# Performance work log

Measured on AMD Instinct MI355X. Metric: run time of the kernel, lower is better.

## Reference

```python
import jax, jax.numpy as jnp
import numpy as np

B, D, H, W = 2, 256, 64, 64
NH = 4
EPS = 1e-5


def _ln(x, g, b):
    # LayerNorm over channel dim of NCHW tensor (matches permute->LN(C)->permute)
    mu = jnp.mean(x, axis=1, keepdims=True)
    var = jnp.mean((x - mu) ** 2, axis=1, keepdims=True)
    xn = (x - mu) * jax.lax.rsqrt(var + EPS)
    return xn * g[None, :, None, None] + b[None, :, None, None]


def _conv1x1(x, w, b):
    # w: (out_c, in_c)
    return jnp.einsum('bchw,oc->bohw', x, w) + b[None, :, None, None]


def _dwconv3x3(x, w, b):
    # depthwise 3x3, w: (C, 1, 3, 3)
    y = jax.lax.conv_general_dilated(
        x, w, window_strides=(1, 1), padding='SAME',
        dimension_numbers=('NCHW', 'OIHW', 'NCHW'), feature_group_count=D)
    return y + b[None, :, None, None]


def setup_inputs() -> dict:
    key = jax.random.key(0)
    ks = jax.random.split(key, 12)
    sc = 0.02

    def n(k, shape):
        return jax.random.normal(k, shape, dtype=jnp.float32) * sc

    return {
        'image_embedding': jax.random.normal(ks[0], (B, D, H, W), dtype=jnp.float32),
        'guide': jax.random.normal(ks[1], (B, D, H, W), dtype=jnp.float32),
        'ln1_g': jnp.ones((D,), jnp.float32), 'ln1_b': jnp.zeros((D,), jnp.float32),
        'ln2_g': jnp.ones((D,), jnp.float32), 'ln2_b': jnp.zeros((D,), jnp.float32),
        'qw1': n(ks[2], (D, D)), 'qb1': jnp.zeros((D,), jnp.float32),
        'qw2': n(ks[3], (D, 1, 3, 3)), 'qb2': jnp.zeros((D,), jnp.float32),
        'kw1': n(ks[4], (D, D)), 'kb1': jnp.zeros((D,), jnp.float32),
        'kw2': n(ks[5], (D, 1, 3, 3)), 'kb2': jnp.zeros((D,), jnp.float32),
        'vw1': n(ks[6], (D, D)), 'vb1': jnp.zeros((D,), jnp.float32),
        'vw2': n(ks[7], (D, 1, 3, 3)), 'vb2': jnp.zeros((D,), jnp.float32),
        'ow': n(ks[8], (D, D)), 'ob': jnp.zeros((D,), jnp.float32),
    }


def reference(image_embedding, guide, ln1_g, ln1_b, ln2_g, ln2_b,
              qw1, qb1, qw2, qb2, kw1, kb1, kw2, kb2,
              vw1, vb1, vw2, vb2, ow, ob):
    residual = image_embedding
    x = _ln(image_embedding, ln1_g, ln1_b)
    g = _ln(guide, ln2_g, ln2_b)

    q = _dwconv3x3(_conv1x1(x, qw1, qb1), qw2, qb2)
    k = _dwconv3x3(_conv1x1(g, kw1, kb1), kw2, kb2)
    v = _dwconv3x3(_conv1x1(g, vw1, vb1), vw2, vb2)

    hd = D // NH
    scale = hd ** -0.5

    def to_heads(t):  # (B,C,H,W) -> (B, NH, HW, hd)
        return t.reshape(B, NH, hd, H * W).transpose(0, 1, 3, 2)

    q = to_heads(q) * scale
    k = to_heads(k)
    v = to_heads(v)

    attn = jax.nn.softmax(jnp.einsum('bhnd,bhmd->bhnm', q, k), axis=-1)
    out = jnp.einsum('bhnm,bhmd->bhnd', attn, v)
    out = out.transpose(0, 1, 3, 2).reshape(B, D, H, W)
    out = _conv1x1(out, ow, ob)
    return residual + out
```

## Files before the change

kernel.cpp:

```cpp
#include <hip/hip_runtime.h>
#include <cstdint>
#include <cstddef>

typedef unsigned short u16;
typedef unsigned int u32;
typedef __attribute__((ext_vector_type(8))) short short8;
typedef __attribute__((ext_vector_type(4))) float f32x4;

#define CD 256
#define HWD 4096
#define NHD 4
#define HDD 64

static __device__ __forceinline__ u16 f2b(float f) {
    u32 u = __builtin_bit_cast(u32, f);
    return (u16)((u + 0x7fffu + ((u >> 16) & 1u)) >> 16);
}
static __device__ __forceinline__ float b2f(u16 h) {
    return __builtin_bit_cast(float, (u32)h << 16);
}
static __device__ __forceinline__ u32 pk2(float a, float b) {
    return (u32)f2b(a) | ((u32)f2b(b) << 16);
}
static __device__ __forceinline__ u32 pk2r(float a, float b) {
    u32 ua = __builtin_bit_cast(u32, a) + 0x8000u;
    u32 ub = __builtin_bit_cast(u32, b) + 0x8000u;
    return (ua >> 16) | (ub & 0xffff0000u);
}
static __device__ __forceinline__ float fexp2(float x) {
#if __has_builtin(__builtin_amdgcn_exp2f)
    return __builtin_amdgcn_exp2f(x);
#else
    return __expf(x * 0.69314718056f);
#endif
}
static __device__ __forceinline__ void async16(const void* g, void* l) {
    __builtin_amdgcn_global_load_lds(
        (const __attribute__((address_space(1))) unsigned int*)g,
        (__attribute__((address_space(3))) unsigned int*)l,
        16, 0, 0);
}

__global__ __launch_bounds__(256) void ln_transpose(
    const float* __restrict__ x0, const float* __restrict__ x1,
    const float* __restrict__ g0, const float* __restrict__ b0,
    const float* __restrict__ g1, const float* __restrict__ b1,
    u16* __restrict__ out0, u16* __restrict__ out1)
{
    int bid = blockIdx.x;
    int t = bid >> 8, b = (bid >> 7) & 1, p0 = (bid & 127) << 5;
    const float* x = t ? x1 : x0;
    const float* g = t ? g1 : g0;
    const float* bb = t ? b1 : b0;
    u16* out = t ? out1 : out0;

    int tid = threadIdx.x;
    int tx = tid & 31, ty = tid >> 5;
    const float* xb = x + (size_t)b * CD * HWD + p0 + tx;

    __shared__ float red[2][8][32];
    __shared__ u16 T[256][33];

    float s = 0.f, sq = 0.f;
    #pragma unroll 8
    for (int i = 0; i < 32; ++i) {
        float v = xb[(size_t)(ty * 32 + i) * HWD];
        s += v; sq += v * v;
    }
    red[0][ty][tx] = s; red[1][ty][tx] = sq;
    __syncthreads();
    float st = 0.f, sqt = 0.f;
    #pragma unroll
    for (int j = 0; j < 8; ++j) { st += red[0][j][tx]; sqt += red[1][j][tx]; }
    float mean = st * (1.f / 256.f);
    float var = sqt * (1.f / 256.f) - mean * mean;
    float rstd = rsqrtf(var + 1e-5f);

    #pragma unroll 8
    for (int i = 0; i < 32; ++i) {
        int c = ty * 32 + i;
        float v = (xb[(size_t)c * HWD] - mean) * rstd * g[c] + bb[c];
        T[c][tx] = f2b(v);
    }
    __syncthreads();

    #pragma unroll
    for (int pass = 0; pass < 4; ++pass) {
        int idx = pass * 256 + tid;
        int p = idx >> 5, cs = (idx & 31) * 8;
        u16 tmp[8];
        #pragma unroll
        for (int j = 0; j < 8; ++j) tmp[j] = T[cs + j][p];
        *(uint4*)&out[((size_t)b * HWD + p0 + p) * CD + cs] = *(const uint4*)tmp;
    }
}

__global__ __launch_bounds__(256) void qkv_gemm(
    const u16* __restrict__ xT, const u16* __restrict__ gT,
    const float* __restrict__ qw1, const float* __restrict__ qb1,
    const float* __restrict__ kw1, const float* __restrict__ kb1,
    const float* __restrict__ vw1, const float* __restrict__ vb1,
    u16* __restrict__ q1, u16* __restrict__ k1, u16* __restrict__ v1)
{
    int z = blockIdx.z;
    int mm = z >> 1, b = z & 1;
    const u16* X    = (mm == 0) ? xT : gT;
    const float* W  = (mm == 0) ? qw1 : (mm == 1) ? kw1 : vw1;
    const float* Bi = (mm == 0) ? qb1 : (mm == 1) ? kb1 : vb1;
    u16* Y          = (mm == 0) ? q1 : (mm == 1) ? k1 : v1;

    int n0 = blockIdx.x * 128;
    int p0 = blockIdx.y * 64;

    __shared__ u16 As[64][40];
    __shared__ u16 Bs[128][40];

    int tid = threadIdx.x;
    int lane = tid & 63, w = tid >> 6;
    int wm = w >> 1, wn = w & 1;
    int l15 = lane & 15, quad = lane >> 4;

    f32x4 acc[2][4];
    #pragma unroll
    for (int mi = 0; mi < 2; ++mi)
        #pragma unroll
        for (int nj = 0; nj < 4; ++nj)
            acc[mi][nj] = (f32x4){0.f, 0.f, 0.f, 0.f};

    const u16* Xb = X + (size_t)b * HWD * CD;

    int arow = tid >> 2, aseg = (tid & 3) * 8;
    const u16* agp = Xb + (size_t)(p0 + arow) * CD + aseg;
    int brow = tid >> 1, bkh = (tid & 1) * 16;
    const float* wgp = W + (size_t)(n0 + brow) * CD + bkh;

    uint4 ra = *(const uint4*)(agp);
    float4 rw0 = ((const float4*)wgp)[0], rw1 = ((const float4*)wgp)[1];
    float4 rw2 = ((const float4*)wgp)[2], rw3 = ((const float4*)wgp)[3];

    for (int kt = 0; kt < 8; ++kt) {
        __syncthreads();
        *(uint4*)&As[arow][aseg] = ra;
        {
            uint4 qa, qb;
            qa.x = pk2(rw0.x, rw0.y); qa.y = pk2(rw0.z, rw0.w);
            qa.z = pk2(rw1.x, rw1.y); qa.w = pk2(rw1.z, rw1.w);
            qb.x = pk2(rw2.x, rw2.y); qb.y = pk2(rw2.z, rw2.w);
            qb.z = pk2(rw3.x, rw3.y); qb.w = pk2(rw3.z, rw3.w);
            *(uint4*)&Bs[brow][bkh] = qa;
            *(uint4*)&Bs[brow][bkh + 8] = qb;
        }
        if (kt < 7) {
            ra = *(const uint4*)(agp + (kt + 1) * 32);
            const float* wg2 = wgp + (kt + 1) * 32;
            rw0 = ((const float4*)wg2)[0]; rw1 = ((const float4*)wg2)[1];
            rw2 = ((const float4*)wg2)[2]; rw3 = ((const float4*)wg2)[3];
        }
        __syncthreads();

        short8 af[2], bf[4];
        #pragma unroll
        for (int mi = 0; mi < 2; ++mi)
            af[mi] = *(const short8*)&As[wm * 32 + mi * 16 + l15][quad * 8];
        #pragma unroll
        for (int nj = 0; nj < 4; ++nj)
            bf[nj] = *(const short8*)&Bs[wn * 64 + nj * 16 + l15][quad * 8];
        #pragma unroll
        for (int mi = 0; mi < 2; ++mi)
            #pragma unroll
            for (int nj = 0; nj < 4; ++nj)
                acc[mi][nj] = __builtin_amdgcn_mfma_f32_16x16x32_bf16(
                    af[mi], bf[nj], acc[mi][nj], 0, 0, 0);
    }

    u16* Yb = Y + (size_t)b * HWD * CD;
    float bias[4];
    #pragma unroll
    for (int nj = 0; nj < 4; ++nj)
        bias[nj] = Bi[n0 + wn * 64 + nj * 16 + l15];
    #pragma unroll
    for (int mi = 0; mi < 2; ++mi) {
        #pragma unroll
        for (int r = 0; r < 4; ++r) {
            int p = p0 + wm * 32 + mi * 16 + quad * 4 + r;
            #pragma unroll
            for (int nj = 0; nj < 4; ++nj) {
                int ch = n0 + wn * 64 + nj * 16 + l15;
                Yb[(size_t)p * CD + ch] = f2b(acc[mi][nj][r] + bias[nj]);
            }
        }
    }
}

__global__ __launch_bounds__(256) void dwconv_nc(
    const u16* __restrict__ q1, const u16* __restrict__ k1, const u16* __restrict__ v1,
    const float* __restrict__ qw2, const float* __restrict__ qb2,
    const float* __restrict__ kw2, const float* __restrict__ kb2,
    const float* __restrict__ vw2, const float* __restrict__ vb2,
    u16* __restrict__ Q, u16* __restrict__ K, u16* __restrict__ Vt)
{
    int bid = blockIdx.x;
    int which = bid >> 9;
    int b = (bid >> 8) & 1;
    int p0 = (bid & 255) * 16;

    const u16* in = ((which == 0) ? q1 : (which == 1) ? k1 : v1) + (size_t)b * HWD * CD;
    const float* wsrc = (which == 0) ? qw2 : (which == 1) ? kw2 : vw2;
    const float* bsrc = (which == 0) ? qb2 : (which == 1) ? kb2 : vb2;
    float oscale = (which == 0) ? 0.18033688011112042f : 1.0f;

    int c = threadIdx.x;
    float w9[9];
    #pragma unroll
    for (int j = 0; j < 9; ++j) w9[j] = wsrc[c * 9 + j];
    float bias = bsrc[c];

    int h = p0 >> 6, w0 = p0 & 63;

    float accv[16];
    #pragma unroll
    for (int pi = 0; pi < 16; ++pi) accv[pi] = bias;

    #pragma unroll
    for (int dh = 0; dh < 3; ++dh) {
        int hh = h + dh - 1;
        if (hh < 0 || hh >= 64) continue;
        const u16* rp = in + ((size_t)hh * 64) * CD + c;
        float r[18];
        r[0] = (w0 > 0) ? b2f(rp[(size_t)(w0 - 1) * CD]) : 0.f;
        #pragma unroll
        for (int j = 1; j <= 16; ++j)
            r[j] = b2f(rp[(size_t)(w0 - 1 + j) * CD]);
        r[17] = (w0 < 48) ? b2f(rp[(size_t)(w0 + 16) * CD]) : 0.f;

        float wa = w9[dh * 3 + 0], wb = w9[dh * 3 + 1], wc = w9[dh * 3 + 2];
        #pragma unroll
        for (int pi = 0; pi < 16; ++pi)
            accv[pi] += wa * r[pi] + wb * r[pi + 1] + wc * r[pi + 2];
    }

    if (which == 2) {
        u32 w8[8];
        #pragma unroll
        for (int j = 0; j < 8; ++j) w8[j] = pk2(accv[2 * j], accv[2 * j + 1]);
        uint4* dst = (uint4*)(Vt + ((size_t)(b * CD + c)) * HWD + p0);
        dst[0] = make_uint4(w8[0], w8[1], w8[2], w8[3]);
        dst[1] = make_uint4(w8[4], w8[5], w8[6], w8[7]);
    } else {
        u16* out = ((which == 0) ? Q : K) + (size_t)b * HWD * CD;
        #pragma unroll
        for (int pi = 0; pi < 16; ++pi)
            out[(size_t)(p0 + pi) * CD + c] = f2b(accv[pi] * oscale);
    }
}

__global__ __launch_bounds__(256, 2) void attn_kernel(
    const u16* __restrict__ Q, const u16* __restrict__ K,
    const u16* __restrict__ Vt, u16* __restrict__ Opart,
    float* __restrict__ Psum)
{
    int qt = blockIdx.x;
    int bh = blockIdx.y;
    int ks = blockIdx.z;
    int b = bh >> 2, nh = bh & 3;

    __shared__ u16 Ks_[2][64 * 64];
    __shared__ u16 Vs_[2][64 * 64];
    __shared__ u16 Ps[256 * 64];

    int tid = threadIdx.x;
    int lane = tid & 63, w = tid >> 6;
    int l15 = lane & 15, quad = lane >> 4;
    int sw = l15 & 7;

    const u16* Qb = Q + ((size_t)b * HWD) * CD + nh * 64;
    const u16* Kb = K + ((size_t)b * HWD) * CD + nh * 64;
    const u16* Vb = Vt + ((size_t)bh * HDD) * HWD;

    short8 qf[4][2];
    #pragma unroll
    for (int qi = 0; qi < 4; ++qi) {
        const u16* qrow = Qb + (size_t)(qt * 256 + w * 64 + qi * 16 + l15) * CD + quad * 8;
        qf[qi][0] = *(const short8*)(qrow);
        qf[qi][1] = *(const short8*)(qrow + 32);
    }

    int rr = lane >> 3;
    int gseg = (lane & 7) ^ rr;
    const u16* kgb = Kb + (size_t)(ks * 1024 + w * 16 + rr) * CD + gseg * 8;
    const u16* vgb = Vb + (size_t)(w * 16 + rr) * HWD + ks * 1024 + gseg * 8;

    f32x4 acc_o[4][4];
    float psum[4] = {0.f, 0.f, 0.f, 0.f};
    #pragma unroll
    for (int qi = 0; qi < 4; ++qi)
        #pragma unroll
        for (int dj = 0; dj < 4; ++dj)
            acc_o[qi][dj] = (f32x4){0.f, 0.f, 0.f, 0.f};

    #pragma unroll
    for (int j = 0; j < 2; ++j) {
        async16(kgb + (size_t)(j * 8) * CD, &Ks_[0][(w * 16 + j * 8) * 64]);
        async16(vgb + (size_t)(j * 8) * HWD, &Vs_[0][(w * 16 + j * 8) * 64]);
    }

    for (int it = 0; it < 16; ++it) {
        int cur = it & 1;
        __syncthreads();
        if (it + 1 < 16) {
            int nxt = cur ^ 1;
            #pragma unroll
            for (int j = 0; j < 2; ++j) {
                async16(kgb + (size_t)((it + 1) * 64 + j * 8) * CD,
                        &Ks_[nxt][(w * 16 + j * 8) * 64]);
                async16(vgb + (size_t)(j * 8) * HWD + (it + 1) * 64,
                        &Vs_[nxt][(w * 16 + j * 8) * 64]);
            }
        }

        short8 kf[4][2];
        #pragma unroll
        for (int nj = 0; nj < 4; ++nj)
            #pragma unroll
            for (int kk = 0; kk < 2; ++kk)
                kf[nj][kk] = *(const short8*)&Ks_[cur][(nj * 16 + l15) * 64 +
                                                      (((kk * 4 + quad) ^ sw) << 3)];

        #pragma unroll
        for (int qi = 0; qi < 4; ++qi) {
            f32x4 st[4];
            #pragma unroll
            for (int nj = 0; nj < 4; ++nj) st[nj] = (f32x4){0.f, 0.f, 0.f, 0.f};
            #pragma unroll
            for (int kk = 0; kk < 2; ++kk)
                #pragma unroll
                for (int nj = 0; nj < 4; ++nj)
                    st[nj] = __builtin_amdgcn_mfma_f32_16x16x32_bf16(
                        kf[nj][kk], qf[qi][kk], st[nj], 0, 0, 0);

            int prow = (w * 64 + qi * 16 + l15) * 64;
            #pragma unroll
            for (int nj = 0; nj < 4; ++nj) {
                float e0 = fexp2(st[nj][0]);
                float e1 = fexp2(st[nj][1]);
                float e2 = fexp2(st[nj][2]);
                float e3 = fexp2(st[nj][3]);
                psum[qi] += (e0 + e1) + (e2 + e3);
                uint2 pw;
                pw.x = pk2r(e0, e1);
                pw.y = pk2r(e2, e3);
                int pcol = (((nj * 2 + (quad >> 1)) ^ sw) << 3) + (quad & 1) * 4;
                *(uint2*)&Ps[prow + pcol] = pw;
            }
        }

        short8 vf[4][2];
        #pragma unroll
        for (int dj = 0; dj < 4; ++dj)
            #pragma unroll
            for (int kk = 0; kk < 2; ++kk)
                vf[dj][kk] = *(const short8*)&Vs_[cur][(dj * 16 + l15) * 64 +
                                                      (((kk * 4 + quad) ^ sw) << 3)];

        #pragma unroll
        for (int kk = 0; kk < 2; ++kk)
            #pragma unroll
            for (int qi = 0; qi < 4; ++qi) {
                short8 pf = *(const short8*)&Ps[(w * 64 + qi * 16 + l15) * 64 +
                                                (((kk * 4 + quad) ^ sw) << 3)];
                #pragma unroll
                for (int dj = 0; dj < 4; ++dj)
                    acc_o[qi][dj] = __builtin_amdgcn_mfma_f32_16x16x32_bf16(
                        pf, vf[dj][kk], acc_o[qi][dj], 0, 0, 0);
            }
    }

    u16* Ob = Opart + (((size_t)ks * 8 + bh) * HWD) * HDD;
    #pragma unroll
    for (int qi = 0; qi < 4; ++qi)
        #pragma unroll
        for (int dj = 0; dj < 4; ++dj)
            #pragma unroll
            for (int r = 0; r < 4; ++r) {
                int n = qt * 256 + w * 64 + qi * 16 + quad * 4 + r;
                Ob[(size_t)n * HDD + dj * 16 + l15] = f2b(acc_o[qi][dj][r]);
            }

    float* Pb = Psum + ((size_t)ks * 8 + bh) * HWD + qt * 256 + w * 64;
    #pragma unroll
    for (int qi = 0; qi < 4; ++qi) {
        float s = psum[qi];
        s += __shfl_xor(s, 16);
        s += __shfl_xor(s, 32);
        if (quad == 0) Pb[qi * 16 + l15] = s;
    }
}

__global__ __launch_bounds__(256) void out_gemm(
    const float* __restrict__ W, const float* __restrict__ Bi,
    const u16* __restrict__ Opart, const float* __restrict__ Psum,
    const float* __restrict__ residual, float* __restrict__ out)
{
    int b = blockIdx.z;
    int m0 = blockIdx.y * 64;
    int n0 = blockIdx.x * 64;

    __shared__ u16 As[64][40];
    __shared__ u16 Bs[64][40];

    int tid = threadIdx.x;
    int lane = tid & 63, w = tid >> 6;
    int wm = w >> 1, wn = w & 1;
    int l15 = lane & 15, quad = lane >> 4;

    f32x4 acc[2][2];
    #pragma unroll
    for (int mi = 0; mi < 2; ++mi)
        #pragma unroll
        for (int nj = 0; nj < 2; ++nj)
            acc[mi][nj] = (f32x4){0.f, 0.f, 0.f, 0.f};

    int arow = tid >> 2, aseg = (tid & 3) * 8;
    const float* wgp = W + (size_t)(m0 + arow) * CD + aseg;
    int brow = tid >> 2, bseg = (tid & 3) * 8;
    int pn = n0 + brow;

    float4 rw0 = ((const float4*)wgp)[0], rw1 = ((const float4*)wgp)[1];

    uint4 ro[4]; float rinv;
    {
        int c = bseg;
        int bh = b * 4 + (c >> 6), d0 = c & 63;
        float p = 0.f;
        #pragma unroll
        for (int s = 0; s < 4; ++s) {
            ro[s] = *(const uint4*)&Opart[(((size_t)s * 8 + bh) * HWD + pn) * HDD + d0];
            p += Psum[((size_t)s * 8 + bh) * HWD + pn];
        }
        rinv = 1.f / p;
    }

    for (int kt = 0; kt < 8; ++kt) {
        __syncthreads();
        {
            uint4 qa;
            qa.x = pk2(rw0.x, rw0.y); qa.y = pk2(rw0.z, rw0.w);
            qa.z = pk2(rw1.x, rw1.y); qa.w = pk2(rw1.z, rw1.w);
            *(uint4*)&As[arow][aseg] = qa;
        }
        {
            float v[8];
            #pragma unroll
            for (int j = 0; j < 8; ++j) v[j] = 0.f;
            #pragma unroll
            for (int s = 0; s < 4; ++s) {
                u16 t[8];
                *(uint4*)t = ro[s];
                #pragma unroll
                for (int j = 0; j < 8; ++j) v[j] += b2f(t[j]);
            }
            uint4 bb;
            bb.x = pk2(v[0] * rinv, v[1] * rinv);
            bb.y = pk2(v[2] * rinv, v[3] * rinv);
            bb.z = pk2(v[4] * rinv, v[5] * rinv);
            bb.w = pk2(v[6] * rinv, v[7] * rinv);
            *(uint4*)&Bs[brow][bseg] = bb;
        }
        if (kt < 7) {
            const float* wg2 = wgp + (kt + 1) * 32;
            rw0 = ((const float4*)wg2)[0]; rw1 = ((const float4*)wg2)[1];
            int c = (kt + 1) * 32 + bseg;
            int bh = b * 4 + (c >> 6), d0 = c & 63;
            float p = 0.f;
            #pragma unroll
            for (int s = 0; s < 4; ++s) {
                ro[s] = *(const uint4*)&Opart[(((size_t)s * 8 + bh) * HWD + pn) * HDD + d0];
                p += Psum[((size_t)s * 8 + bh) * HWD + pn];
            }
            rinv = 1.f / p;
        }
        __syncthreads();

        short8 af[2], bf[2];
        #pragma unroll
        for (int mi = 0; mi < 2; ++mi)
            af[mi] = *(const short8*)&As[wm * 32 + mi * 16 + l15][quad * 8];
        #pragma unroll
        for (int nj = 0; nj < 2; ++nj)
            bf[nj] = *(const short8*)&Bs[wn * 32 + nj * 16 + l15][quad * 8];
        #pragma unroll
        for (int mi = 0; mi < 2; ++mi)
            #pragma unroll
            for (int nj = 0; nj < 2; ++nj)
                acc[mi][nj] = __builtin_amdgcn_mfma_f32_16x16x32_bf16(
                    af[mi], bf[nj], acc[mi][nj], 0, 0, 0);
    }

    #pragma unroll
    for (int mi = 0; mi < 2; ++mi) {
        int mb = m0 + wm * 32 + mi * 16 + quad * 4;
        #pragma unroll
        for (int r = 0; r < 4; ++r) {
            float bias = Bi[mb + r];
            const float* res = residual + (size_t)(b * CD + mb + r) * HWD;
            float* o = out + (size_t)(b * CD + mb + r) * HWD;
            #pragma unroll
            for (int nj = 0; nj < 2; ++nj) {
                int n = n0 + wn * 32 + nj * 16 + l15;
                o[n] = acc[mi][nj][r] + bias + res[n];
            }
        }
    }
}

extern "C" void kernel_launch(void* const* d_in, const int* in_sizes, int n_in,
                              void* d_out, int out_size, void* d_ws, size_t ws_size,
                              hipStream_t stream) {
    (void)in_sizes; (void)n_in; (void)out_size; (void)ws_size;

    const float* image = (const float*)d_in[0];
    const float* guide = (const float*)d_in[1];
    const float* ln1_g = (const float*)d_in[2];
    const float* ln1_b = (const float*)d_in[3];
    const float* ln2_g = (const float*)d_in[4];
    const float* ln2_b = (const float*)d_in[5];
    const float* qw1 = (const float*)d_in[6];
    const float* qb1 = (const float*)d_in[7];
    const float* qw2 = (const float*)d_in[8];
    const float* qb2 = (const float*)d_in[9];
    const float* kw1 = (const float*)d_in[10];
    const float* kb1 = (const float*)d_in[11];
    const float* kw2 = (const float*)d_in[12];
    const float* kb2 = (const float*)d_in[13];
    const float* vw1 = (const float*)d_in[14];
    const float* vb1 = (const float*)d_in[15];
    const float* vw2 = (const float*)d_in[16];
    const float* vb2 = (const float*)d_in[17];
    const float* ow  = (const float*)d_in[18];
    const float* ob  = (const float*)d_in[19];
    float* out = (float*)d_out;

    char* ws = (char*)d_ws;
    u16* xT    = (u16*)(ws + (size_t)0  * (1 << 20));
    u16* gT    = (u16*)(ws + (size_t)4  * (1 << 20));
    u16* q1    = (u16*)(ws + (size_t)8  * (1 << 20));
    u16* k1    = (u16*)(ws + (size_t)12 * (1 << 20));
    u16* v1    = (u16*)(ws + (size_t)16 * (1 << 20));
    u16* Qh    = (u16*)(ws + (size_t)20 * (1 << 20));
    u16* Kh    = (u16*)(ws + (size_t)24 * (1 << 20));
    u16* Vt    = (u16*)(ws + (size_t)28 * (1 << 20));
    u16*   Opart = (u16*)(ws + (size_t)0  * (1 << 20));
    float* Psum  = (float*)(ws + (size_t)18 * (1 << 20));

    ln_transpose<<<dim3(512), dim3(256), 0, stream>>>(
        image, guide, ln1_g, ln1_b, ln2_g, ln2_b, xT, gT);

    qkv_gemm<<<dim3(2, 64, 6), dim3(256), 0, stream>>>(
        xT, gT, qw1, qb1, kw1, kb1, vw1, vb1, q1, k1, v1);

    dwconv_nc<<<dim3(1536), dim3(256), 0, stream>>>(
        q1, k1, v1, qw2, qb2, kw2, kb2, vw2, vb2, Qh, Kh, Vt);

    attn_kernel<<<dim3(16, 8, 4), dim3(256), 0, stream>>>(Qh, Kh, Vt, Opart, Psum);

    out_gemm<<<dim3(64, 4, 2), dim3(256), 0, stream>>>(
        ow, ob, Opart, Psum, image, out);
}
```

Before: 182.1 us.

## Switch attention to 32x32 MFMA with register-resident P via permlane swap

Rewrites the attention inner loop to use 32x32x16 bf16 MFMAs, with each wave owning 32 query rows instead of 64. The exponentiated scores are converted with v_cvt_pk_bf16_f32 and rearranged with permlane32_swap, so they feed the PV MFMA straight from registers and the LDS P staging buffer is gone. Dropping the 32KB P buffer and using fewer query rows per block allows four blocks per CU and doubles the grid. In exchange, K/V tiles are reloaded from global memory by twice as many blocks, and correctness depends on the swapped lane layout matching the MFMA operand layout.

```diff
diff --git a/kernel.cpp b/kernel.cpp
--- a/kernel.cpp
+++ b/kernel.cpp
@@ -6,6 +6,8 @@
 typedef unsigned int u32;
 typedef __attribute__((ext_vector_type(8))) short short8;
 typedef __attribute__((ext_vector_type(4))) float f32x4;
+typedef __attribute__((ext_vector_type(16))) float f32x16;
+typedef __attribute__((ext_vector_type(2))) unsigned int u32x2;
 
 #define CD 256
 #define HWD 4096
@@ -21,11 +23,6 @@
 }
 static __device__ __forceinline__ u32 pk2(float a, float b) {
     return (u32)f2b(a) | ((u32)f2b(b) << 16);
-}
-static __device__ __forceinline__ u32 pk2r(float a, float b) {
-    u32 ua = __builtin_bit_cast(u32, a) + 0x8000u;
-    u32 ub = __builtin_bit_cast(u32, b) + 0x8000u;
-    return (ua >> 16) | (ub & 0xffff0000u);
 }
 static __device__ __forceinline__ float fexp2(float x) {
 #if __has_builtin(__builtin_amdgcn_exp2f)
@@ -33,6 +30,14 @@
 #else
     return __expf(x * 0.69314718056f);
 #endif
+}
+static __device__ __forceinline__ u32 cvtpk(float lo, float hi) {
+    u32 r;
+    asm("v_cvt_pk_bf16_f32 %0, %1, %2" : "=v"(r) : "v"(lo), "v"(hi));
+    return r;
+}
+static __device__ __forceinline__ u32x2 plswap(u32 a, u32 b) {
+    return __builtin_amdgcn_permlane32_swap(a, b, false, false);
 }
 static __device__ __forceinline__ void async16(const void* g, void* l) {
     __builtin_amdgcn_global_load_lds(
@@ -254,7 +259,7 @@
     }
 }
 
-__global__ __launch_bounds__(256, 2) void attn_kernel(
+__global__ __launch_bounds__(256, 4) void attn_kernel(
     const u16* __restrict__ Q, const u16* __restrict__ K,
     const u16* __restrict__ Vt, u16* __restrict__ Opart,
     float* __restrict__ Psum)
@@ -266,37 +271,34 @@
 
     __shared__ u16 Ks_[2][64 * 64];
     __shared__ u16 Vs_[2][64 * 64];
-    __shared__ u16 Ps[256 * 64];
 
     int tid = threadIdx.x;
     int lane = tid & 63, w = tid >> 6;
-    int l15 = lane & 15, quad = lane >> 4;
-    int sw = l15 & 7;
+    int l31 = lane & 31, h = lane >> 5;
+    int sw = l31 & 7;
 
     const u16* Qb = Q + ((size_t)b * HWD) * CD + nh * 64;
     const u16* Kb = K + ((size_t)b * HWD) * CD + nh * 64;
     const u16* Vb = Vt + ((size_t)bh * HDD) * HWD;
 
-    short8 qf[4][2];
-    #pragma unroll
-    for (int qi = 0; qi < 4; ++qi) {
-        const u16* qrow = Qb + (size_t)(qt * 256 + w * 64 + qi * 16 + l15) * CD + quad * 8;
-        qf[qi][0] = *(const short8*)(qrow);
-        qf[qi][1] = *(const short8*)(qrow + 32);
-    }
+    int q0 = qt * 128 + w * 32;
+
+    short8 qf[4];
+    #pragma unroll
+    for (int si = 0; si < 4; ++si)
+        qf[si] = *(const short8*)(Qb + (size_t)(q0 + l31) * CD + si * 16 + h * 8);
 
     int rr = lane >> 3;
     int gseg = (lane & 7) ^ rr;
     const u16* kgb = Kb + (size_t)(ks * 1024 + w * 16 + rr) * CD + gseg * 8;
     const u16* vgb = Vb + (size_t)(w * 16 + rr) * HWD + ks * 1024 + gseg * 8;
 
-    f32x4 acc_o[4][4];
-    float psum[4] = {0.f, 0.f, 0.f, 0.f};
-    #pragma unroll
-    for (int qi = 0; qi < 4; ++qi)
-        #pragma unroll
-        for (int dj = 0; dj < 4; ++dj)
-            acc_o[qi][dj] = (f32x4){0.f, 0.f, 0.f, 0.f};
+    f32x16 acc[2];
+    #pragma unroll
+    for (int db = 0; db < 2; ++db)
+        #pragma unroll
+        for (int r = 0; r < 16; ++r) acc[db][r] = 0.f;
+    float psum = 0.f;
 
     #pragma unroll
     for (int j = 0; j < 2; ++j) {
@@ -318,82 +320,65 @@
             }
         }
 
-        short8 kf[4][2];
-        #pragma unroll
-        for (int nj = 0; nj < 4; ++nj)
-            #pragma unroll
-            for (int kk = 0; kk < 2; ++kk)
-                kf[nj][kk] = *(const short8*)&Ks_[cur][(nj * 16 + l15) * 64 +
-                                                      (((kk * 4 + quad) ^ sw) << 3)];
-
-        #pragma unroll
-        for (int qi = 0; qi < 4; ++qi) {
-            f32x4 st[4];
-            #pragma unroll
-            for (int nj = 0; nj < 4; ++nj) st[nj] = (f32x4){0.f, 0.f, 0.f, 0.f};
-            #pragma unroll
-            for (int kk = 0; kk < 2; ++kk)
-                #pragma unroll
-                for (int nj = 0; nj < 4; ++nj)
-                    st[nj] = __builtin_amdgcn_mfma_f32_16x16x32_bf16(
-                        kf[nj][kk], qf[qi][kk], st[nj], 0, 0, 0);
-
-            int prow = (w * 64 + qi * 16 + l15) * 64;
-            #pragma unroll
-            for (int nj = 0; nj < 4; ++nj) {
-                float e0 = fexp2(st[nj][0]);
-                float e1 = fexp2(st[nj][1]);
-                float e2 = fexp2(st[nj][2]);
-                float e3 = fexp2(st[nj][3]);
-                psum[qi] += (e0 + e1) + (e2 + e3);
-                uint2 pw;
-                pw.x = pk2r(e0, e1);
-                pw.y = pk2r(e2, e3);
-                int pcol = (((nj * 2 + (quad >> 1)) ^ sw) << 3) + (quad & 1) * 4;
-                *(uint2*)&Ps[prow + pcol] = pw;
+        #pragma unroll
+        for (int kb = 0; kb < 2; ++kb) {
+            short8 kf[4];
+            #pragma unroll
+            for (int si = 0; si < 4; ++si)
+                kf[si] = *(const short8*)&Ks_[cur][(kb * 32 + l31) * 64 +
+                                                   (((si * 2 + h) ^ sw) << 3)];
+            f32x16 st;
+            #pragma unroll
+            for (int r = 0; r < 16; ++r) st[r] = 0.f;
+            #pragma unroll
+            for (int si = 0; si < 4; ++si)
+                st = __builtin_amdgcn_mfma_f32_32x32x16_bf16(
+                    kf[si], qf[si], st, 0, 0, 0);
+
+            float e[16];
+            #pragma unroll
+            for (int r = 0; r < 16; ++r) e[r] = fexp2(st[r]);
+            #pragma unroll
+            for (int r = 0; r < 16; r += 4)
+                psum += (e[r] + e[r + 1]) + (e[r + 2] + e[r + 3]);
+
+            u32 wv[8];
+            #pragma unroll
+            for (int m = 0; m < 8; ++m) wv[m] = cvtpk(e[2 * m], e[2 * m + 1]);
+            u32x2 s02 = plswap(wv[0], wv[2]);
+            u32x2 s13 = plswap(wv[1], wv[3]);
+            u32x2 s46 = plswap(wv[4], wv[6]);
+            u32x2 s57 = plswap(wv[5], wv[7]);
+            union { u32 u[4]; short8 s8; } p0_, p1_;
+            p0_.u[0] = s02.x; p0_.u[1] = s13.x; p0_.u[2] = s02.y; p0_.u[3] = s13.y;
+            p1_.u[0] = s46.x; p1_.u[1] = s57.x; p1_.u[2] = s46.y; p1_.u[3] = s57.y;
+
+            #pragma unroll
+            for (int db = 0; db < 2; ++db) {
+                short8 vf0 = *(const short8*)&Vs_[cur][(db * 32 + l31) * 64 +
+                                 ((((kb * 2 + 0) * 2 + h) ^ sw) << 3)];
+                acc[db] = __builtin_amdgcn_mfma_f32_32x32x16_bf16(
+                    p0_.s8, vf0, acc[db], 0, 0, 0);
+                short8 vf1 = *(const short8*)&Vs_[cur][(db * 32 + l31) * 64 +
+                                 ((((kb * 2 + 1) * 2 + h) ^ sw) << 3)];
+                acc[db] = __builtin_amdgcn_mfma_f32_32x32x16_bf16(
+                    p1_.s8, vf1, acc[db], 0, 0, 0);
             }
         }
-
-        short8 vf[4][2];
-        #pragma unroll
-        for (int dj = 0; dj < 4; ++dj)
-            #pragma unroll
-            for (int kk = 0; kk < 2; ++kk)
-                vf[dj][kk] = *(const short8*)&Vs_[cur][(dj * 16 + l15) * 64 +
-                                                      (((kk * 4 + quad) ^ sw) << 3)];
-
-        #pragma unroll
-        for (int kk = 0; kk < 2; ++kk)
-            #pragma unroll
-            for (int qi = 0; qi < 4; ++qi) {
-                short8 pf = *(const short8*)&Ps[(w * 64 + qi * 16 + l15) * 64 +
-                                                (((kk * 4 + quad) ^ sw) << 3)];
-                #pragma unroll
-                for (int dj = 0; dj < 4; ++dj)
-                    acc_o[qi][dj] = __builtin_amdgcn_mfma_f32_16x16x32_bf16(
-                        pf, vf[dj][kk], acc_o[qi][dj], 0, 0, 0);
-            }
     }
 
     u16* Ob = Opart + (((size_t)ks * 8 + bh) * HWD) * HDD;
     #pragma unroll
-    for (int qi = 0; qi < 4; ++qi)
-        #pragma unroll
-        for (int dj = 0; dj < 4; ++dj)
-            #pragma unroll
-            for (int r = 0; r < 4; ++r) {
-                int n = qt * 256 + w * 64 + qi * 16 + quad * 4 + r;
-                Ob[(size_t)n * HDD + dj * 16 + l15] = f2b(acc_o[qi][dj][r]);
-            }
-
-    float* Pb = Psum + ((size_t)ks * 8 + bh) * HWD + qt * 256 + w * 64;
-    #pragma unroll
-    for (int qi = 0; qi < 4; ++qi) {
-        float s = psum[qi];
-        s += __shfl_xor(s, 16);
-        s += __shfl_xor(s, 32);
-        if (quad == 0) Pb[qi * 16 + l15] = s;
-    }
+    for (int db = 0; db < 2; ++db)
+        #pragma unroll
+        for (int r = 0; r < 16; ++r) {
+            int n = q0 + (r & 3) + 8 * (r >> 2) + 4 * h;
+            Ob[(size_t)n * HDD + db * 32 + l31] = f2b(acc[db][r]);
+        }
+
+    float s = psum + __shfl_xor(psum, 32);
+    float* Pb = Psum + ((size_t)ks * 8 + bh) * HWD + q0;
+    if (lane < 32) Pb[lane] = s;
 }
 
 __global__ __launch_bounds__(256) void out_gemm(
@@ -561,7 +546,7 @@
     dwconv_nc<<<dim3(1536), dim3(256), 0, stream>>>(
         q1, k1, v1, qw2, qb2, kw2, kb2, vw2, vb2, Qh, Kh, Vt);
 
-    attn_kernel<<<dim3(16, 8, 4), dim3(256), 0, stream>>>(Qh, Kh, Vt, Opart, Psum);
+    attn_kernel<<<dim3(32, 8, 4), dim3(256), 0, stream>>>(Qh, Kh, Vt, Opart, Psum);
 
     out_gemm<<<dim3(64, 4, 2), dim3(256), 0, stream>>>(
         ow, ob, Opart, Psum, image, out);
```

New measurement: 185.9 us. 2.1% more time.
